# Performance work log

Hardware: AMD Instinct MI355X
Metric: run time of the kernel (lower is better)

Reference implementation:

```python
import jax, jax.numpy as jnp
import numpy as np

P, IMG, CH, DM, NL = 16, 224, 3, 512, 6
DI, N, K, R = 2 * DM, 16, 4, DM // 16  # d_inner, d_state, d_conv, dt_rank
BATCH = 32
L = (IMG // P) ** 2
PD = CH * P * P


def layernorm(x, g, b, eps=1e-5):
    mu = x.mean(-1, keepdims=True)
    var = x.var(-1, keepdims=True)
    return (x - mu) / jnp.sqrt(var + eps) * g + b


def mamba_layer(x, inW, convW, convB, xpW, dtW, dtB, A_log, Dvec, outW):
    # x: (B, L, DM)
    Bsz, Ls, _ = x.shape
    xz = x @ inW.T                      # (B, L, 2*DI), in_proj (bias=False)
    xs, z = jnp.split(xz, 2, axis=-1)   # (B, L, DI) each
    # causal depthwise conv1d (kernel K, left pad K-1, truncate to L)
    xp = jnp.pad(xs, ((0, 0), (K - 1, 0), (0, 0)))
    xc = sum(convW[:, k] * xp[:, k:k + Ls, :] for k in range(K)) + convB
    xc = jax.nn.silu(xc)
    # input-dependent dt, B, C
    x_dbl = xc @ xpW.T                  # (B, L, R + 2N)
    dt, Bm, Cm = jnp.split(x_dbl, [R, R + N], axis=-1)
    dt = jax.nn.softplus(dt @ dtW.T + dtB)  # (B, L, DI)
    A = -jnp.exp(A_log)                 # (DI, N)

    def step(h, inp):
        xt, dtt, Bt, Ct = inp           # (B,DI),(B,DI),(B,N),(B,N)
        dA = jnp.exp(dtt[:, :, None] * A)              # (B, DI, N)
        h = dA * h + dtt[:, :, None] * Bt[:, None, :] * xt[:, :, None]
        y = jnp.einsum('bdn,bn->bd', h, Ct)
        return h, y

    h0 = jnp.zeros((Bsz, DI, N), xs.dtype)
    xs_t = jnp.swapaxes(xc, 0, 1)
    dt_t = jnp.swapaxes(dt, 0, 1)
    B_t = jnp.swapaxes(Bm, 0, 1)
    C_t = jnp.swapaxes(Cm, 0, 1)
    _, ys = jax.lax.scan(step, h0, (xs_t, dt_t, B_t, C_t))
    y = jnp.swapaxes(ys, 0, 1) + xc * Dvec   # skip term D*x
    y = y * jax.nn.silu(z)
    return y @ outW.T                    # out_proj (bias=False)


def setup_inputs() -> dict:
    key = jax.random.key(0)
    ks = jax.random.split(key, 16)
    s = 0.02
    inp = {
        'x': jax.random.normal(ks[0], (BATCH, CH, IMG, IMG), jnp.float32),
        'ln0_g': jnp.ones((PD,), jnp.float32),
        'ln0_b': jnp.zeros((PD,), jnp.float32),
        'W_emb': jax.random.normal(ks[1], (DM, PD), jnp.float32) * s,
        'b_emb': jnp.zeros((DM,), jnp.float32),
        'ln1_g': jnp.ones((DM,), jnp.float32),
        'ln1_b': jnp.zeros((DM,), jnp.float32),
        'in_proj_w': jax.random.normal(ks[2], (NL, 2 * DI, DM), jnp.float32) * s,
        'conv_w': jax.random.normal(ks[3], (NL, DI, K), jnp.float32) * 0.1,
        'conv_b': jnp.zeros((NL, DI), jnp.float32),
        'x_proj_w': jax.random.normal(ks[4], (NL, R + 2 * N, DI), jnp.float32) * s,
        'dt_proj_w': jax.random.normal(ks[5], (NL, DI, R), jnp.float32) * s,
        'dt_proj_b': jnp.full((NL, DI), float(np.log(np.expm1(0.01))), jnp.float32),
        'A_log': jnp.tile(jnp.log(jnp.arange(1, N + 1, dtype=jnp.float32)), (NL, DI, 1)),
        'D_p': jnp.ones((NL, DI), jnp.float32),
        'out_proj_w': jax.random.normal(ks[6], (NL, DM, DI), jnp.float32) * s,
        'blk_ln_g': jnp.ones((NL, DM), jnp.float32),
        'blk_ln_b': jnp.zeros((NL, DM), jnp.float32),
        'W_head': jax.random.normal(ks[7], (10, DM), jnp.float32) * s,
        'b_head': jnp.zeros((10,), jnp.float32),
    }
    return inp


def reference(x, ln0_g, ln0_b, W_emb, b_emb, ln1_g, ln1_b, in_proj_w, conv_w,
              conv_b, x_proj_w, dt_proj_w, dt_proj_b, A_log, D_p, out_proj_w,
              blk_ln_g, blk_ln_b, W_head, b_head):
    B = x.shape[0]
    # patchify: b c (h p1) (w p2) -> b (h w) (c p1 p2)
    g = IMG // P
    t = x.reshape(B, CH, g, P, g, P).transpose(0, 2, 4, 1, 3, 5).reshape(B, g * g, PD)
    t = layernorm(t, ln0_g, ln0_b)
    t = t @ W_emb.T + b_emb
    t = layernorm(t, ln1_g, ln1_b)
    for i in range(NL):
        y = mamba_layer(t, in_proj_w[i], conv_w[i], conv_b[i], x_proj_w[i],
                        dt_proj_w[i], dt_proj_b[i], A_log[i], D_p[i], out_proj_w[i])
        t = layernorm(y + t, blk_ln_g[i], blk_ln_b[i])
    pooled = t.mean(axis=1)
    return pooled @ W_head.T + b_head
```

## Files before the change

### kernel.cpp

```cpp
#include <hip/hip_runtime.h>
#include <cstdint>
#include <cstddef>

#define BATCHN 32
#define LSEQ   196
#define DMODEL 512
#define DINNER 1024
#define PDIM   768
#define NSTATE 16
#define RRANK  32
#define NLAYER 6

typedef __bf16 bf16_t;
typedef __bf16 bf16x8 __attribute__((ext_vector_type(8)));
typedef float  f32x4  __attribute__((ext_vector_type(4)));

__device__ __forceinline__ void gl_lds16(const bf16_t* g, bf16_t* l) {
    __builtin_amdgcn_global_load_lds(
        (const __attribute__((address_space(1))) void*)g,
        (__attribute__((address_space(3))) void*)l, 16, 0, 0);
}

__global__ __launch_bounds__(256) void split_kernel(
    const float* __restrict__ src, bf16_t* __restrict__ hi,
    bf16_t* __restrict__ lo, int n)
{
    int i = blockIdx.x * 256 + threadIdx.x;
    if (i < n) {
        float x = src[i];
        bf16_t h = (bf16_t)x;
        hi[i] = h;
        lo[i] = (bf16_t)(x - (float)h);
    }
}

__global__ __launch_bounds__(256) void gemm_mfma3(
    const bf16_t* __restrict__ Ah, const bf16_t* __restrict__ Al,
    const bf16_t* __restrict__ Wh, const bf16_t* __restrict__ Wl,
    float* __restrict__ C, const float* __restrict__ bias,
    int M, int N, int K)
{
    __shared__ bf16_t sAh[128 * 32];
    __shared__ bf16_t sAl[128 * 32];
    __shared__ bf16_t sBh[2][128 * 32];
    __shared__ bf16_t sBl[2][128 * 32];

    const int bm = blockIdx.y * 128;
    const int bn = blockIdx.x * 128;
    const int kchunk = K / gridDim.z;
    const int kb = blockIdx.z * kchunk;
    C += (size_t)blockIdx.z * M * N;

    const int tid  = threadIdx.x;
    const int lane = tid & 63;
    const int w    = tid >> 6;
    const int wm   = (w & 1) * 64;
    const int wn   = (w >> 1) * 64;

    const int lrow = lane >> 2;
    const int cg8  = ((lane & 3) ^ ((lane >> 3) & 3)) * 8;
    const size_t arow = (size_t)(bm + w * 32 + lrow) * K + cg8;
    const size_t brow = (size_t)(bn + w * 32 + lrow) * K + cg8;

    const int fsw = ((lane >> 4) ^ ((lane >> 1) & 3)) * 8;
    const int fr  = lane & 15;
    const int llo = w * 1024;

    f32x4 acc[4][4] = {};

    #pragma unroll
    for (int j = 0; j < 2; ++j) {
        gl_lds16(Ah + arow + (size_t)j * 16 * K + kb, &sAh[llo + j * 512]);
        gl_lds16(Al + arow + (size_t)j * 16 * K + kb, &sAl[llo + j * 512]);
        gl_lds16(Wh + brow + (size_t)j * 16 * K + kb, &sBh[0][llo + j * 512]);
        gl_lds16(Wl + brow + (size_t)j * 16 * K + kb, &sBl[0][llo + j * 512]);
    }

    const int kiter = kchunk / 32;
    for (int ki = 0; ki < kiter; ++ki) {
        const int buf = ki & 1;
        __syncthreads();

        bf16x8 afh[4], afl[4];
        #pragma unroll
        for (int mt = 0; mt < 4; ++mt) {
            const int r = wm + mt * 16 + fr;
            afh[mt] = *(const bf16x8*)&sAh[r * 32 + fsw];
            afl[mt] = *(const bf16x8*)&sAl[r * 32 + fsw];
        }
        __syncthreads();

        if (ki + 1 < kiter) {
            const int k0 = kb + (ki + 1) * 32;
            #pragma unroll
            for (int j = 0; j < 2; ++j) {
                gl_lds16(Ah + arow + (size_t)j * 16 * K + k0, &sAh[llo + j * 512]);
                gl_lds16(Al + arow + (size_t)j * 16 * K + k0, &sAl[llo + j * 512]);
                gl_lds16(Wh + brow + (size_t)j * 16 * K + k0, &sBh[buf ^ 1][llo + j * 512]);
                gl_lds16(Wl + brow + (size_t)j * 16 * K + k0, &sBl[buf ^ 1][llo + j * 512]);
            }
        }

        bf16x8 bfh[4], bfl[4];
        #pragma unroll
        for (int nt = 0; nt < 4; ++nt) {
            const int r = wn + nt * 16 + fr;
            bfh[nt] = *(const bf16x8*)&sBh[buf][r * 32 + fsw];
            bfl[nt] = *(const bf16x8*)&sBl[buf][r * 32 + fsw];
        }
        #pragma unroll
        for (int nt = 0; nt < 4; ++nt)
            #pragma unroll
            for (int mt = 0; mt < 4; ++mt)
                acc[mt][nt] = __builtin_amdgcn_mfma_f32_16x16x32_bf16(
                    afh[mt], bfh[nt], acc[mt][nt], 0, 0, 0);
        #pragma unroll
        for (int nt = 0; nt < 4; ++nt)
            #pragma unroll
            for (int mt = 0; mt < 4; ++mt)
                acc[mt][nt] = __builtin_amdgcn_mfma_f32_16x16x32_bf16(
                    afh[mt], bfl[nt], acc[mt][nt], 0, 0, 0);
        #pragma unroll
        for (int nt = 0; nt < 4; ++nt)
            #pragma unroll
            for (int mt = 0; mt < 4; ++mt)
                acc[mt][nt] = __builtin_amdgcn_mfma_f32_16x16x32_bf16(
                    afl[mt], bfh[nt], acc[mt][nt], 0, 0, 0);
    }

    const int cr = (lane >> 4) * 4;
    const int cc = lane & 15;
    #pragma unroll
    for (int nt = 0; nt < 4; ++nt) {
        const int n = bn + wn + nt * 16 + cc;
        const float bv = bias ? bias[n] : 0.f;
        #pragma unroll
        for (int mt = 0; mt < 4; ++mt) {
            const int m0 = bm + wm + mt * 16 + cr;
            #pragma unroll
            for (int r = 0; r < 4; ++r)
                C[(size_t)(m0 + r) * N + n] = acc[mt][nt][r] + bv;
        }
    }
}

__global__ __launch_bounds__(256) void gemm_nt(
    const float* __restrict__ A, int lda,
    const float* __restrict__ W,
    float* __restrict__ C, int ldc,
    const float* __restrict__ bias,
    int M, int N, int K, int act)
{
    __shared__ float As[16][64];
    __shared__ float Ws[16][64];
    const int bm = blockIdx.y * 64;
    const int bn = blockIdx.x * 64;
    const int tid = threadIdx.x;
    const int tx = tid & 15;
    const int ty = tid >> 4;
    const int r   = tid >> 2;
    const int kk4 = (tid & 3) << 2;

    float acc[4][4];
    #pragma unroll
    for (int i = 0; i < 4; ++i)
        #pragma unroll
        for (int j = 0; j < 4; ++j) acc[i][j] = 0.f;

    for (int k0 = 0; k0 < K; k0 += 16) {
        float4 va = *(const float4*)(A + (size_t)(bm + r) * lda + k0 + kk4);
        float4 vw = *(const float4*)(W + (size_t)(bn + r) * K   + k0 + kk4);
        __syncthreads();
        As[kk4 + 0][r] = va.x; As[kk4 + 1][r] = va.y;
        As[kk4 + 2][r] = va.z; As[kk4 + 3][r] = va.w;
        Ws[kk4 + 0][r] = vw.x; Ws[kk4 + 1][r] = vw.y;
        Ws[kk4 + 2][r] = vw.z; Ws[kk4 + 3][r] = vw.w;
        __syncthreads();
        #pragma unroll
        for (int kk = 0; kk < 16; ++kk) {
            float4 a = *(const float4*)&As[kk][ty << 2];
            float4 b = *(const float4*)&Ws[kk][tx << 2];
            acc[0][0] += a.x * b.x; acc[0][1] += a.x * b.y;
            acc[0][2] += a.x * b.z; acc[0][3] += a.x * b.w;
            acc[1][0] += a.y * b.x; acc[1][1] += a.y * b.y;
            acc[1][2] += a.y * b.z; acc[1][3] += a.y * b.w;
            acc[2][0] += a.z * b.x; acc[2][1] += a.z * b.y;
            acc[2][2] += a.z * b.z; acc[2][3] += a.z * b.w;
            acc[3][0] += a.w * b.x; acc[3][1] += a.w * b.y;
            acc[3][2] += a.w * b.z; acc[3][3] += a.w * b.w;
        }
    }

    #pragma unroll
    for (int i = 0; i < 4; ++i) {
        const int m = bm + (ty << 2) + i;
        #pragma unroll
        for (int j = 0; j < 4; ++j) {
            const int n = bn + (tx << 2) + j;
            float v = acc[i][j];
            if (bias) v += bias[n];
            if (act == 1) {
                v = (v > 20.f) ? v : log1pf(expf(v));
            }
            C[(size_t)m * ldc + n] = v;
        }
    }
}

__global__ __launch_bounds__(256) void conv_xproj_kernel(
    const float* __restrict__ xz, const float* __restrict__ cw,
    const float* __restrict__ cb, const float* __restrict__ xpW,
    float* __restrict__ xc, float* __restrict__ Cpart,
    int kchunk)
{
    __shared__ float As[16][64];
    __shared__ float Ws[16][64];
    __shared__ float scw[128 * 4 + 128];

    const int bm = blockIdx.y * 64;
    const int kb = blockIdx.z * kchunk;
    Cpart += (size_t)blockIdx.z * (BATCHN * LSEQ) * 64;

    const int tid = threadIdx.x;
    if (tid < 128) {
        *(float4*)&scw[tid * 4] = *(const float4*)(cw + (size_t)(kb + tid) * 4);
        scw[512 + tid] = cb[kb + tid];
    }
    __syncthreads();

    const int tx = tid & 15;
    const int ty = tid >> 4;
    const int r   = tid >> 2;
    const int kk4 = (tid & 3) << 2;
    const int bl  = bm + r;
    const int l   = bl % LSEQ;
    const float* xrow = xz + ((size_t)bl << 11);

    float acc[4][4];
    #pragma unroll
    for (int i = 0; i < 4; ++i)
        #pragma unroll
        for (int j = 0; j < 4; ++j) acc[i][j] = 0.f;

    for (int k0 = 0; k0 < kchunk; k0 += 16) {
        const int cl = k0 + kk4;
        const int c  = kb + cl;
        float4 va = *(const float4*)&scw[512 + cl];
        #pragma unroll
        for (int kk = 0; kk < 4; ++kk) {
            int ls = l + kk - 3;
            if (ls >= 0) {
                float4 xv = *(const float4*)(xrow + ((ptrdiff_t)(kk - 3) << 11) + c);
                va.x += scw[(cl + 0) * 4 + kk] * xv.x;
                va.y += scw[(cl + 1) * 4 + kk] * xv.y;
                va.z += scw[(cl + 2) * 4 + kk] * xv.z;
                va.w += scw[(cl + 3) * 4 + kk] * xv.w;
            }
        }
        va.x = va.x * __builtin_amdgcn_rcpf(1.f + __expf(-va.x));
        va.y = va.y * __builtin_amdgcn_rcpf(1.f + __expf(-va.y));
        va.z = va.z * __builtin_amdgcn_rcpf(1.f + __expf(-va.z));
        va.w = va.w * __builtin_amdgcn_rcpf(1.f + __expf(-va.w));
        *(float4*)(xc + ((size_t)bl << 10) + c) = va;

        float4 vw = *(const float4*)(xpW + (size_t)r * DINNER + c);
        __syncthreads();
        As[kk4 + 0][r] = va.x; As[kk4 + 1][r] = va.y;
        As[kk4 + 2][r] = va.z; As[kk4 + 3][r] = va.w;
        Ws[kk4 + 0][r] = vw.x; Ws[kk4 + 1][r] = vw.y;
        Ws[kk4 + 2][r] = vw.z; Ws[kk4 + 3][r] = vw.w;
        __syncthreads();
        #pragma unroll
        for (int kk = 0; kk < 16; ++kk) {
            float4 a = *(const float4*)&As[kk][ty << 2];
            float4 b = *(const float4*)&Ws[kk][tx << 2];
            acc[0][0] += a.x * b.x; acc[0][1] += a.x * b.y;
            acc[0][2] += a.x * b.z; acc[0][3] += a.x * b.w;
            acc[1][0] += a.y * b.x; acc[1][1] += a.y * b.y;
            acc[1][2] += a.y * b.z; acc[1][3] += a.y * b.w;
            acc[2][0] += a.z * b.x; acc[2][1] += a.z * b.y;
            acc[2][2] += a.z * b.z; acc[2][3] += a.z * b.w;
            acc[3][0] += a.w * b.x; acc[3][1] += a.w * b.y;
            acc[3][2] += a.w * b.z; acc[3][3] += a.w * b.w;
        }
    }

    #pragma unroll
    for (int i = 0; i < 4; ++i) {
        const int m = bm + (ty << 2) + i;
        #pragma unroll
        for (int j = 0; j < 4; ++j) {
            const int n = (tx << 2) + j;
            Cpart[(size_t)m * 64 + n] = acc[i][j];
        }
    }
}

__global__ __launch_bounds__(256) void reduce_splitk(
    const float* __restrict__ part, float* __restrict__ out, int n, int nsplit)
{
    int i = blockIdx.x * 256 + threadIdx.x;
    if (i < n) {
        float s = 0.f;
        for (int j = 0; j < nsplit; ++j) s += part[(size_t)j * n + i];
        out[i] = s;
    }
}

__global__ __launch_bounds__(256) void patchify_kernel(
    const float* __restrict__ x, float* __restrict__ tp)
{
    int idx = blockIdx.x * 256 + threadIdx.x;
    int pd = idx % PDIM;
    int bl = idx / PDIM;
    int l = bl % LSEQ, b = bl / LSEQ;
    int c = pd >> 8, rem = pd & 255, p1 = rem >> 4, p2 = rem & 15;
    int gh = l / 14, gw = l % 14;
    int hh = gh * 16 + p1, ww = gw * 16 + p2;
    tp[idx] = x[(((size_t)b * 3 + c) * 224 + hh) * 224 + ww];
}

__global__ __launch_bounds__(256) void ln_kernel(
    const float* __restrict__ in, const float* __restrict__ in2,
    const float* __restrict__ res,
    const float* __restrict__ g, const float* __restrict__ bt,
    float* __restrict__ out, bf16_t* __restrict__ hi,
    bf16_t* __restrict__ lo, int W)
{
    __shared__ float red[4];
    const int row = blockIdx.x;
    const size_t base = (size_t)row * W;
    const int nper = W >> 8;
    float vals[3];
    float s = 0.f;
    for (int j = 0; j < nper; ++j) {
        int c = (j << 8) + threadIdx.x;
        float v = in[base + c];
        if (in2) v += in2[base + c];
        if (res) v += res[base + c];
        vals[j] = v;
        s += v;
    }
    int lane = threadIdx.x & 63, wid = threadIdx.x >> 6;
    #pragma unroll
    for (int o = 32; o > 0; o >>= 1) s += __shfl_down(s, o);
    if (lane == 0) red[wid] = s;
    __syncthreads();
    float mu = (red[0] + red[1] + red[2] + red[3]) / (float)W;
    __syncthreads();
    float vs = 0.f;
    for (int j = 0; j < nper; ++j) { float d = vals[j] - mu; vs += d * d; }
    #pragma unroll
    for (int o = 32; o > 0; o >>= 1) vs += __shfl_down(vs, o);
    if (lane == 0) red[wid] = vs;
    __syncthreads();
    float var = (red[0] + red[1] + red[2] + red[3]) / (float)W;
    float rstd = rsqrtf(var + 1e-5f);
    for (int j = 0; j < nper; ++j) {
        int c = (j << 8) + threadIdx.x;
        float v = (vals[j] - mu) * rstd * g[c] + bt[c];
        if (out) out[base + c] = v;
        if (hi) {
            bf16_t h = (bf16_t)v;
            hi[base + c] = h;
            lo[base + c] = (bf16_t)(v - (float)h);
        }
    }
}

template<int J>
__device__ __forceinline__ float qbcast(float v) {
    constexpr int ctrl = J | (J << 2) | (J << 4) | (J << 6);
    return __int_as_float(__builtin_amdgcn_mov_dpp(
        __float_as_int(v), ctrl, 0xF, 0xF, true));
}

__global__ __launch_bounds__(256, 1) void scan_kernel(
    const float* __restrict__ xc, const float* __restrict__ dt,
    const float* __restrict__ xdbl, const float* __restrict__ A_log,
    const float* __restrict__ Dv, const float* __restrict__ xz,
    bf16_t* __restrict__ yh, bf16_t* __restrict__ yl)
{
    __shared__ float sBC[4][2][256];

    const int b    = blockIdx.y;
    const int tid  = threadIdx.x;
    const int lane = tid & 63;
    const int w    = tid >> 6;
    const int q    = tid >> 2;
    const int sub  = tid & 3;
    const int d    = blockIdx.x * 64 + q;

    float A2[4], h[4];
    #pragma unroll
    for (int n = 0; n < 4; ++n) {
        A2[n] = -__expf(A_log[d * NSTATE + sub * 4 + n]) * 1.44269504f;
        h[n] = 0.f;
    }
    const float Dval = Dv[d];
    const size_t bL = (size_t)b * LSEQ;

    const float* pdt = dt + (bL + sub) * DINNER + d;
    const float* pxc = xc + (bL + sub) * DINNER + d;
    const float* pz  = xz + ((bL + sub) << 11) + DINNER + d;

    const float* xrow = xdbl + bL * 64;
    const int roff = (lane >> 4) * 64 + (lane & 15) * 4;
    float* lds0 = &sBC[w][0][0];
    float* lds1 = &sBC[w][1][0];

    float4 r0 = *(const float4*)(xrow + roff);
    float4 r1 = *(const float4*)(xrow + 256 + roff);
    float4 rowreg = *(const float4*)(xrow + 512 + roff);
    *(float4*)(lds0 + roff) = r0;
    *(float4*)(lds1 + roff) = r1;

    float dt_c = pdt[0];          float xc_c = pxc[0];          float z_c = pz[0];
    float dt_1 = pdt[4 * DINNER]; float xc_1 = pxc[4 * DINNER]; float z_1 = pz[4 * 2048];

    for (int g = 0; g < 49; ++g) {
        const int gl  = (g + 3 <= 48) ? g + 3 : 48;
        float4 rownext = *(const float4*)(xrow + gl * 256 + roff);
        const int adv = (g < 47) ? 2 : (48 - g);
        float dt_2 = pdt[(size_t)adv * 4 * DINNER];
        float xc_2 = pxc[(size_t)adv * 4 * DINNER];
        float z_2  = pz[(size_t)adv * 4 * 2048];

        const float* Bbuf = (g & 1) ? lds1 : lds0;
        float acc_keep = 0.f;

#define SCAN_STEP(J) do {                                                     \
        float4 Bv = *(const float4*)&Bbuf[(J) * 64 + 32 + 4 * sub];           \
        float4 Cv = *(const float4*)&Bbuf[(J) * 64 + 48 + 4 * sub];           \
        float dtv = qbcast<J>(dt_c);                                          \
        float xv  = qbcast<J>(xc_c);                                          \
        float dtx = dtv * xv;                                                 \
        h[0] = exp2f(dtv * A2[0]) * h[0] + dtx * Bv.x;                        \
        h[1] = exp2f(dtv * A2[1]) * h[1] + dtx * Bv.y;                        \
        h[2] = exp2f(dtv * A2[2]) * h[2] + dtx * Bv.z;                        \
        h[3] = exp2f(dtv * A2[3]) * h[3] + dtx * Bv.w;                        \
        float acc = h[0] * Cv.x + h[1] * Cv.y + h[2] * Cv.z + h[3] * Cv.w;    \
        acc += __shfl_xor(acc, 1);                                            \
        acc += __shfl_xor(acc, 2);                                            \
        acc_keep = (sub == (J)) ? acc : acc_keep;                             \
    } while (0)

        SCAN_STEP(0);
        SCAN_STEP(1);
        SCAN_STEP(2);
        SCAN_STEP(3);
#undef SCAN_STEP

        {
            float yv = acc_keep + xc_c * Dval;
            float sz = z_c * __builtin_amdgcn_rcpf(1.f + __expf(-z_c));
            float o  = yv * sz;
            bf16_t ho = (bf16_t)o;
            const size_t oi = (bL + 4 * (size_t)g + sub) * DINNER + d;
            yh[oi] = ho;
            yl[oi] = (bf16_t)(o - (float)ho);
        }

        *(float4*)(((g & 1) ? lds1 : lds0) + roff) = rowreg;
        rowreg = rownext;

        pdt += 4 * DINNER; pxc += 4 * DINNER; pz += 4 * 2048;
        dt_c = dt_1; xc_c = xc_1; z_c = z_1;
        dt_1 = dt_2; xc_1 = xc_2; z_1 = z_2;
    }
}

__global__ __launch_bounds__(256) void pool_kernel(
    const float* __restrict__ t, float* __restrict__ pooled)
{
    int idx = blockIdx.x * 256 + threadIdx.x;
    int dm = idx & (DMODEL - 1);
    int b = idx >> 9;
    float s = 0.f;
    for (int l = 0; l < LSEQ; ++l)
        s += t[((size_t)(b * LSEQ + l) << 9) + dm];
    pooled[idx] = s * (1.f / (float)LSEQ);
}

__global__ __launch_bounds__(320) void head_kernel(
    const float* __restrict__ pooled, const float* __restrict__ Wh,
    const float* __restrict__ bh, float* __restrict__ out)
{
    int tid = threadIdx.x;
    if (tid >= 320) return;
    int b = tid / 10, o = tid % 10;
    float s = bh[o];
    for (int k = 0; k < DMODEL; ++k)
        s += pooled[b * DMODEL + k] * Wh[o * DMODEL + k];
    out[b * 10 + o] = s;
}

extern "C" void kernel_launch(void* const* d_in, const int* in_sizes, int n_in,
                              void* d_out, int out_size, void* d_ws, size_t ws_size,
                              hipStream_t stream)
{
    const float* x         = (const float*)d_in[0];
    const float* ln0_g     = (const float*)d_in[1];
    const float* ln0_b     = (const float*)d_in[2];
    const float* W_emb     = (const float*)d_in[3];
    const float* b_emb     = (const float*)d_in[4];
    const float* ln1_g     = (const float*)d_in[5];
    const float* ln1_b     = (const float*)d_in[6];
    const float* in_proj_w = (const float*)d_in[7];
    const float* conv_w    = (const float*)d_in[8];
    const float* conv_b    = (const float*)d_in[9];
    const float* x_proj_w  = (const float*)d_in[10];
    const float* dt_proj_w = (const float*)d_in[11];
    const float* dt_proj_b = (const float*)d_in[12];
    const float* A_log     = (const float*)d_in[13];
    const float* D_p       = (const float*)d_in[14];
    const float* out_proj_w= (const float*)d_in[15];
    const float* blk_ln_g  = (const float*)d_in[16];
    const float* blk_ln_b  = (const float*)d_in[17];
    const float* W_head    = (const float*)d_in[18];
    const float* b_head    = (const float*)d_in[19];

    const int M = BATCHN * LSEQ;
    const int NSPLIT = 8;

    char* ws = (char*)d_ws;
    size_t off = 0;
    auto alloc = [&](size_t bytes) -> void* {
        void* p = (void*)(ws + off);
        off += (bytes + 255) & ~(size_t)255;
        return p;
    };
    float*  tp     = (float*)alloc((size_t)M * PDIM * 4);
    bf16_t* tp_h   = (bf16_t*)alloc((size_t)M * PDIM * 2);
    bf16_t* tp_l   = (bf16_t*)alloc((size_t)M * PDIM * 2);
    float*  t      = (float*)alloc((size_t)M * DMODEL * 4);
    bf16_t* t_h    = (bf16_t*)alloc((size_t)M * DMODEL * 2);
    bf16_t* t_l    = (bf16_t*)alloc((size_t)M * DMODEL * 2);
    float*  xz     = (float*)alloc((size_t)M * 2 * DINNER * 4);
    float*  xc     = (float*)alloc((size_t)M * DINNER * 4);
    float*  xdbl   = (float*)alloc((size_t)M * 64 * 4);
    float*  dtbuf  = (float*)alloc((size_t)M * DINNER * 4);
    bf16_t* y_h    = (bf16_t*)alloc((size_t)M * DINNER * 2);
    bf16_t* y_l    = (bf16_t*)alloc((size_t)M * DINNER * 2);
    float*  pooled = (float*)alloc((size_t)BATCHN * DMODEL * 4);
    float*  xdbl_p = tp;
    float*  yout   = dtbuf;
    const int n_inW  = NLAYER * 2 * DINNER * DMODEL;
    const int n_outW = NLAYER * DMODEL * DINNER;
    const int n_embW = DMODEL * PDIM;
    bf16_t* winh  = (bf16_t*)alloc((size_t)n_inW * 2);
    bf16_t* winl  = (bf16_t*)alloc((size_t)n_inW * 2);
    bf16_t* wouth = (bf16_t*)alloc((size_t)n_outW * 2);
    bf16_t* woutl = (bf16_t*)alloc((size_t)n_outW * 2);
    bf16_t* wembh = (bf16_t*)alloc((size_t)n_embW * 2);
    bf16_t* wembl = (bf16_t*)alloc((size_t)n_embW * 2);
    (void)ws_size; (void)in_sizes; (void)n_in; (void)out_size;

    split_kernel<<<(n_inW  + 255) / 256, 256, 0, stream>>>(in_proj_w,  winh,  winl,  n_inW);
    split_kernel<<<(n_outW + 255) / 256, 256, 0, stream>>>(out_proj_w, wouth, woutl, n_outW);
    split_kernel<<<(n_embW + 255) / 256, 256, 0, stream>>>(W_emb,      wembh, wembl, n_embW);

    patchify_kernel<<<(M * PDIM) / 256, 256, 0, stream>>>(x, tp);
    ln_kernel<<<M, 256, 0, stream>>>(tp, nullptr, nullptr, ln0_g, ln0_b,
                                     nullptr, tp_h, tp_l, PDIM);
    gemm_mfma3<<<dim3(DMODEL / 128, M / 128, 1), 256, 0, stream>>>(
        tp_h, tp_l, wembh, wembl, t, b_emb, M, DMODEL, PDIM);
    ln_kernel<<<M, 256, 0, stream>>>(t, nullptr, nullptr, ln1_g, ln1_b,
                                     t, t_h, t_l, DMODEL);

    for (int i = 0; i < NLAYER; ++i) {
        const bf16_t* winh_i  = winh  + (size_t)i * 2 * DINNER * DMODEL;
        const bf16_t* winl_i  = winl  + (size_t)i * 2 * DINNER * DMODEL;
        const bf16_t* wouth_i = wouth + (size_t)i * DMODEL * DINNER;
        const bf16_t* woutl_i = woutl + (size_t)i * DMODEL * DINNER;
        const float* cw   = conv_w    + (size_t)i * DINNER * 4;
        const float* cb   = conv_b    + (size_t)i * DINNER;
        const float* xpW  = x_proj_w  + (size_t)i * 64 * DINNER;
        const float* dtW  = dt_proj_w + (size_t)i * DINNER * RRANK;
        const float* dtB  = dt_proj_b + (size_t)i * DINNER;
        const float* Ali  = A_log     + (size_t)i * DINNER * NSTATE;
        const float* Di   = D_p       + (size_t)i * DINNER;
        const float* bg   = blk_ln_g  + (size_t)i * DMODEL;
        const float* bb   = blk_ln_b  + (size_t)i * DMODEL;

        gemm_mfma3<<<dim3((2 * DINNER) / 128, M / 128, 1), 256, 0, stream>>>(
            t_h, t_l, winh_i, winl_i, xz, nullptr, M, 2 * DINNER, DMODEL);
        conv_xproj_kernel<<<dim3(1, M / 64, NSPLIT), 256, 0, stream>>>(
            xz, cw, cb, xpW, xc, xdbl_p, DINNER / NSPLIT);
        reduce_splitk<<<(M * 64 + 255) / 256, 256, 0, stream>>>(
            xdbl_p, xdbl, M * 64, NSPLIT);
        gemm_nt<<<dim3(DINNER / 64, M / 64), 256, 0, stream>>>(
            xdbl, 64, dtW, dtbuf, DINNER, dtB, M, DINNER, RRANK, 1);
        scan_kernel<<<dim3(DINNER / 64, BATCHN), 256, 0, stream>>>(
            xc, dtbuf, xdbl, Ali, Di, xz, y_h, y_l);
        gemm_mfma3<<<dim3(DMODEL / 128, M / 128, 2), 256, 0, stream>>>(
            y_h, y_l, wouth_i, woutl_i, yout, nullptr, M, DMODEL, DINNER);
        ln_kernel<<<M, 256, 0, stream>>>(yout, yout + (size_t)M * DMODEL, t,
                                         bg, bb, t, t_h, t_l, DMODEL);
    }

    pool_kernel<<<(BATCHN * DMODEL) / 256, 256, 0, stream>>>(t, pooled);
    head_kernel<<<1, 320, 0, stream>>>(pooled, W_head, b_head, (float*)d_out);
}
```

Baseline: 1.530 ms.

## Split scan state across 8 lanes per channel to double scan parallelism

The selective-scan kernel now assigns 8 lanes per inner channel, each holding 2 of the 16 state elements, instead of 4 lanes holding 4 each. The grid doubles to 32 channels per block, and launch bounds allow 4 blocks per CU. Per-step values are broadcast with ds_swizzle, and the reduction gains a DPP half-mirror step. The hi and lo bf16 outputs are written by separate lane halves. The aim is to shorten the serial recurrence work per thread and raise occupancy to hide latency, at the cost of an extra cross-lane reduction per step and duplicated loads of dt, xc and z.

```diff
diff --git a/kernel.cpp b/kernel.cpp
--- a/kernel.cpp
+++ b/kernel.cpp
@@ -369,13 +369,16 @@
 }
 
 template<int J>
-__device__ __forceinline__ float qbcast(float v) {
-    constexpr int ctrl = J | (J << 2) | (J << 4) | (J << 6);
+__device__ __forceinline__ float obcast(float v) {
+    constexpr int offset = (J << 5) | 0x18;
+    return __int_as_float(__builtin_amdgcn_ds_swizzle(__float_as_int(v), offset));
+}
+__device__ __forceinline__ float half_mirror(float v) {
     return __int_as_float(__builtin_amdgcn_mov_dpp(
-        __float_as_int(v), ctrl, 0xF, 0xF, true));
-}
-
-__global__ __launch_bounds__(256, 1) void scan_kernel(
+        __float_as_int(v), 0x141, 0xF, 0xF, true));
+}
+
+__global__ __launch_bounds__(256, 4) void scan_kernel(
     const float* __restrict__ xc, const float* __restrict__ dt,
     const float* __restrict__ xdbl, const float* __restrict__ A_log,
     const float* __restrict__ Dv, const float* __restrict__ xz,
@@ -387,22 +390,22 @@
     const int tid  = threadIdx.x;
     const int lane = tid & 63;
     const int w    = tid >> 6;
-    const int q    = tid >> 2;
-    const int sub  = tid & 3;
-    const int d    = blockIdx.x * 64 + q;
-
-    float A2[4], h[4];
-    #pragma unroll
-    for (int n = 0; n < 4; ++n) {
-        A2[n] = -__expf(A_log[d * NSTATE + sub * 4 + n]) * 1.44269504f;
+    const int sub  = tid & 7;
+    const int s3   = sub & 3;
+    const int d    = blockIdx.x * 32 + (tid >> 3);
+
+    float A2[2], h[2];
+    #pragma unroll
+    for (int n = 0; n < 2; ++n) {
+        A2[n] = -__expf(A_log[d * NSTATE + 2 * sub + n]) * 1.44269504f;
         h[n] = 0.f;
     }
     const float Dval = Dv[d];
     const size_t bL = (size_t)b * LSEQ;
 
-    const float* pdt = dt + (bL + sub) * DINNER + d;
-    const float* pxc = xc + (bL + sub) * DINNER + d;
-    const float* pz  = xz + ((bL + sub) << 11) + DINNER + d;
+    const float* pdt = dt + (bL + s3) * DINNER + d;
+    const float* pxc = xc + (bL + s3) * DINNER + d;
+    const float* pz  = xz + ((bL + s3) << 11) + DINNER + d;
 
     const float* xrow = xdbl + bL * 64;
     const int roff = (lane >> 4) * 64 + (lane & 15) * 4;
@@ -430,19 +433,18 @@
         float acc_keep = 0.f;
 
 #define SCAN_STEP(J) do {                                                     \
-        float4 Bv = *(const float4*)&Bbuf[(J) * 64 + 32 + 4 * sub];           \
-        float4 Cv = *(const float4*)&Bbuf[(J) * 64 + 48 + 4 * sub];           \
-        float dtv = qbcast<J>(dt_c);                                          \
-        float xv  = qbcast<J>(xc_c);                                          \
+        float2 Bv = *(const float2*)&Bbuf[(J) * 64 + 32 + 2 * sub];           \
+        float2 Cv = *(const float2*)&Bbuf[(J) * 64 + 48 + 2 * sub];           \
+        float dtv = obcast<J>(dt_c);                                          \
+        float xv  = obcast<J>(xc_c);                                          \
         float dtx = dtv * xv;                                                 \
         h[0] = exp2f(dtv * A2[0]) * h[0] + dtx * Bv.x;                        \
         h[1] = exp2f(dtv * A2[1]) * h[1] + dtx * Bv.y;                        \
-        h[2] = exp2f(dtv * A2[2]) * h[2] + dtx * Bv.z;                        \
-        h[3] = exp2f(dtv * A2[3]) * h[3] + dtx * Bv.w;                        \
-        float acc = h[0] * Cv.x + h[1] * Cv.y + h[2] * Cv.z + h[3] * Cv.w;    \
+        float acc = h[0] * Cv.x + h[1] * Cv.y;                                \
         acc += __shfl_xor(acc, 1);                                            \
         acc += __shfl_xor(acc, 2);                                            \
-        acc_keep = (sub == (J)) ? acc : acc_keep;                             \
+        acc += half_mirror(acc);                                              \
+        acc_keep = (s3 == (J)) ? acc : acc_keep;                              \
     } while (0)
 
         SCAN_STEP(0);
@@ -456,9 +458,9 @@
             float sz = z_c * __builtin_amdgcn_rcpf(1.f + __expf(-z_c));
             float o  = yv * sz;
             bf16_t ho = (bf16_t)o;
-            const size_t oi = (bL + 4 * (size_t)g + sub) * DINNER + d;
-            yh[oi] = ho;
-            yl[oi] = (bf16_t)(o - (float)ho);
+            const size_t oi = (bL + 4 * (size_t)g + s3) * DINNER + d;
+            if (sub < 4) yh[oi] = ho;
+            else         yl[oi] = (bf16_t)(o - (float)ho);
         }
 
         *(float4*)(((g & 1) ? lds1 : lds0) + roff) = rowreg;
@@ -591,7 +593,7 @@
             xdbl_p, xdbl, M * 64, NSPLIT);
         gemm_nt<<<dim3(DINNER / 64, M / 64), 256, 0, stream>>>(
             xdbl, 64, dtW, dtbuf, DINNER, dtB, M, DINNER, RRANK, 1);
-        scan_kernel<<<dim3(DINNER / 64, BATCHN), 256, 0, stream>>>(
+        scan_kernel<<<dim3(DINNER / 32, BATCHN), 256, 0, stream>>>(
             xc, dtbuf, xdbl, Ali, Di, xz, y_h, y_l);
         gemm_mfma3<<<dim3(DMODEL / 128, M / 128, 2), 256, 0, stream>>>(
             y_h, y_l, wouth_i, woutl_i, yout, nullptr, M, DMODEL, DINNER);
```

Measured after the change: 1.581 ms. 3.3% more time.
